# Optimization experiments

Measured on AMD Instinct MI355X. Metric: run time of the kernel, lower is better.

## Reference

```python
import jax, jax.numpy as jnp
import numpy as np

N = 50000      # nodes
E = 800000     # directed edges (before self-loops)
IN = 128       # in_channels
H = 4          # heads (layers 1,2)
C = 64         # hidden_channels per head
OUT = 512      # out_channels of final Linear
LEAKY_SLOPE = 0.2


def _gat_layer(x, src, dst, n, W, a_src, a_dst, b, concat):
    """PyG GATConv (v1): shared linear, additive attention, segment softmax over dst."""
    heads, ch = a_src.shape
    xl = (x @ W).reshape(n, heads, ch)                       # [N,H,C]
    as_n = jnp.sum(xl * a_src, axis=-1)                      # [N,H] alpha_src per node
    ad_n = jnp.sum(xl * a_dst, axis=-1)                      # [N,H] alpha_dst per node
    logits = jax.nn.leaky_relu(as_n[src] + ad_n[dst], LEAKY_SLOPE)  # [Etot,H]
    m = jax.lax.stop_gradient(jax.ops.segment_max(logits, dst, num_segments=n))
    p = jnp.exp(logits - m[dst])
    denom = jax.ops.segment_sum(p, dst, num_segments=n) + 1e-16
    alpha = p / denom[dst]                                   # segment softmax over incoming edges
    out = jax.ops.segment_sum(xl[src] * alpha[:, :, None], dst, num_segments=n)  # [N,H,C]
    out = out.reshape(n, heads * ch) if concat else out.mean(axis=1)
    return out + b


def setup_inputs() -> dict:
    key = jax.random.key(0)
    ks = jax.random.split(key, 16)

    def gl(k, shape, fan_in):
        return jax.random.normal(k, shape, dtype=jnp.float32) * np.float32(1.0 / np.sqrt(fan_in))

    x = jax.random.normal(ks[0], (N, IN), dtype=jnp.float32)
    edge_index = jax.random.randint(ks[1], (2, E), 0, N, dtype=jnp.int32)

    inp = {
        "x": x,
        "edge_index": edge_index,
        # layer 1: in -> H*C (concat)
        "W1": gl(ks[2], (IN, H * C), IN),
        "a_src1": gl(ks[3], (H, C), C),
        "a_dst1": gl(ks[4], (H, C), C),
        "b1": jnp.zeros((H * C,), jnp.float32),
        # layer 2: H*C -> H*C (concat)
        "W2": gl(ks[5], (H * C, H * C), H * C),
        "a_src2": gl(ks[6], (H, C), C),
        "a_dst2": gl(ks[7], (H, C), C),
        "b2": jnp.zeros((H * C,), jnp.float32),
        # layer 3: H*C -> C (1 head, no concat)
        "W3": gl(ks[8], (H * C, C), H * C),
        "a_src3": gl(ks[9], (1, C), C),
        "a_dst3": gl(ks[10], (1, C), C),
        "b3": jnp.zeros((C,), jnp.float32),
        # final fc: C -> OUT
        "Wfc": gl(ks[11], (C, OUT), C),
        "bfc": jnp.zeros((OUT,), jnp.float32),
    }
    return inp


def reference(x, edge_index, W1, a_src1, a_dst1, b1, W2, a_src2, a_dst2, b2,
              W3, a_src3, a_dst3, b3, Wfc, bfc):
    n = x.shape[0]
    loop = jnp.arange(n, dtype=edge_index.dtype)             # PyG GATConv adds self-loops
    src = jnp.concatenate([edge_index[0], loop])
    dst = jnp.concatenate([edge_index[1], loop])

    h = jax.nn.relu(_gat_layer(x, src, dst, n, W1, a_src1, a_dst1, b1, True))
    h = jax.nn.relu(_gat_layer(h, src, dst, n, W2, a_src2, a_dst2, b2, True))
    h = jax.nn.relu(_gat_layer(h, src, dst, n, W3, a_src3, a_dst3, b3, False))
    return jax.nn.relu(h @ Wfc + bfc)                        # [N, OUT]
```

## Files before the change

kernel.cpp:

```cpp
#include <hip/hip_runtime.h>
#include <cstdint>
#include <cstddef>

typedef unsigned short ushort_t;
typedef __bf16 bf16x8 __attribute__((ext_vector_type(8)));
typedef float f32x4 __attribute__((ext_vector_type(4)));

__device__ __forceinline__ float b2f(ushort_t u) {
    return __uint_as_float(((unsigned int)u) << 16);
}
__device__ __forceinline__ ushort_t f2b(float f) {
    __bf16 h = (__bf16)f;
    return *(ushort_t*)&h;
}
__device__ __forceinline__ float lo16(unsigned int u) { return __uint_as_float(u << 16); }
__device__ __forceinline__ float hi16(unsigned int u) { return __uint_as_float(u & 0xffff0000u); }
__device__ __forceinline__ unsigned int pack2(float a, float b) {
    return ((unsigned int)f2b(b) << 16) | (unsigned int)f2b(a);
}

__device__ __forceinline__ void stage8(const float* __restrict__ g, ushort_t* s) {
    float4 f0 = *(const float4*)g;
    float4 f1 = *(const float4*)(g + 4);
    union { ushort_t u[8]; uint4 v; } t;
    t.u[0] = f2b(f0.x); t.u[1] = f2b(f0.y); t.u[2] = f2b(f0.z); t.u[3] = f2b(f0.w);
    t.u[4] = f2b(f1.x); t.u[5] = f2b(f1.y); t.u[6] = f2b(f1.z); t.u[7] = f2b(f1.w);
    *(uint4*)s = t.v;
}
__device__ __forceinline__ void stage8(const ushort_t* __restrict__ g, ushort_t* s) {
    *(float4*)s = *(const float4*)g;
}

__global__ __launch_bounds__(256) void transpose_kernel(const float* __restrict__ W,
                                                        ushort_t* __restrict__ WT,
                                                        int K, int N2) {
    int id = blockIdx.x * 256 + threadIdx.x;
    if (id >= K * N2) return;
    int n = id / K, k = id - n * K;
    WT[id] = f2b(W[k * N2 + n]);
}

__global__ __launch_bounds__(256) void degree_kernel(const int* __restrict__ ei_dst,
                                                     int* __restrict__ deg, int E, int Etot) {
    int e = blockIdx.x * 256 + threadIdx.x;
    if (e >= Etot) return;
    int d = (e < E) ? ei_dst[e] : (e - E);
    atomicAdd(&deg[d], 1);
}

__global__ __launch_bounds__(256) void partial_sum_kernel(const int* __restrict__ deg,
                                                          int* __restrict__ bsum, int n) {
    __shared__ int ws[4];
    int t = threadIdx.x;
    int i = blockIdx.x * 256 + t;
    int v = (i < n) ? deg[i] : 0;
#pragma unroll
    for (int off = 32; off; off >>= 1) v += __shfl_xor(v, off, 64);
    if ((t & 63) == 0) ws[t >> 6] = v;
    __syncthreads();
    if (t == 0) bsum[blockIdx.x] = ws[0] + ws[1] + ws[2] + ws[3];
}

__global__ __launch_bounds__(256) void scan_bsum_kernel(const int* __restrict__ bsum,
                                                        int* __restrict__ boff,
                                                        int* __restrict__ rowoff,
                                                        int nblk, int n) {
    __shared__ int sm[256];
    int t = threadIdx.x;
    int v = (t < nblk) ? bsum[t] : 0;
    sm[t] = v;
    __syncthreads();
#pragma unroll
    for (int off = 1; off < 256; off <<= 1) {
        int u = (t >= off) ? sm[t - off] : 0;
        __syncthreads();
        sm[t] += u;
        __syncthreads();
    }
    if (t < nblk) boff[t] = sm[t] - v;
    if (t == 255) rowoff[n] = sm[255];
}

__global__ __launch_bounds__(256) void block_scan_kernel(const int* __restrict__ deg,
                                                         const int* __restrict__ boff,
                                                         int* __restrict__ rowoff, int n) {
    __shared__ int sm[256];
    int t = threadIdx.x;
    int i = blockIdx.x * 256 + t;
    int v = (i < n) ? deg[i] : 0;
    sm[t] = v;
    __syncthreads();
#pragma unroll
    for (int off = 1; off < 256; off <<= 1) {
        int u = (t >= off) ? sm[t - off] : 0;
        __syncthreads();
        sm[t] += u;
        __syncthreads();
    }
    if (i < n) rowoff[i] = boff[blockIdx.x] + sm[t] - v;
}

__global__ __launch_bounds__(256) void copy_cursor_kernel(const int* __restrict__ rowoff,
                                                          int* __restrict__ cursor, int n) {
    int i = blockIdx.x * 256 + threadIdx.x;
    if (i < n) cursor[i] = rowoff[i];
}

__global__ __launch_bounds__(256) void scatter_kernel(const int* __restrict__ ei_src,
                                                      const int* __restrict__ ei_dst,
                                                      int* __restrict__ cursor,
                                                      int* __restrict__ ssrc, int E, int Etot) {
    int e = blockIdx.x * 256 + threadIdx.x;
    if (e >= Etot) return;
    int s, d;
    if (e < E) { s = ei_src[e]; d = ei_dst[e]; } else { s = d = e - E; }
    int pos = atomicAdd(&cursor[d], 1);
    ssrc[pos] = s;
}

template <typename TA, bool EPI>
__global__ __launch_bounds__(256) void gemm_mfma(const TA* __restrict__ A,
                                                 const ushort_t* __restrict__ WT,
                                                 float* __restrict__ C,
                                                 ushort_t* __restrict__ Cb,
                                                 const float* __restrict__ bias,
                                                 int M, int K, int N2) {
    __shared__ ushort_t sA[64 * 32];
    __shared__ ushort_t sB[64 * 32];
    const int tid = threadIdx.x;
    const int wv = tid >> 6, lane = tid & 63;
    const int quad = lane >> 4, l16 = lane & 15;
    const int bm = blockIdx.x * 64, bn = blockIdx.y * 64;
    const int srow = tid >> 2, skof = (tid & 3) * 8;
    f32x4 acc[4] = {};

    for (int k0 = 0; k0 < K; k0 += 32) {
        int gm = bm + srow;
        gm = gm < M ? gm : M - 1;
        stage8(A + (size_t)gm * K + k0 + skof, sA + srow * 32 + skof);
        stage8(WT + (size_t)(bn + srow) * K + k0 + skof, sB + srow * 32 + skof);
        __syncthreads();

        bf16x8 af = *(const bf16x8*)(sA + (wv * 16 + l16) * 32 + quad * 8);
#pragma unroll
        for (int j = 0; j < 4; j++) {
            bf16x8 bf = *(const bf16x8*)(sB + (j * 16 + l16) * 32 + quad * 8);
            acc[j] = __builtin_amdgcn_mfma_f32_16x16x32_bf16(af, bf, acc[j], 0, 0, 0);
        }
        __syncthreads();
    }

#pragma unroll
    for (int j = 0; j < 4; j++) {
        int col = bn + j * 16 + l16;
        float bv = EPI ? bias[col] : 0.f;
#pragma unroll
        for (int r = 0; r < 4; r++) {
            int row = bm + wv * 16 + quad * 4 + r;
            if (row < M) {
                float v = acc[j][r];
                if (EPI) {
                    v += bv;
                    v = v > 0.f ? v : 0.f;
                    C[(size_t)row * N2 + col] = v;
                } else {
                    Cb[(size_t)row * N2 + col] = f2b(v);
                }
            }
        }
    }
}

template <int CH>
__global__ __launch_bounds__(256) void attn_kernel(const ushort_t* __restrict__ xl,
                                                   const float* __restrict__ a_src,
                                                   const float* __restrict__ a_dst,
                                                   float* __restrict__ as_n,
                                                   float* __restrict__ ad_n, int N) {
    int n = blockIdx.x * 4 + (threadIdx.x >> 6);
    int lane = threadIdx.x & 63;
    if (n >= N) return;
    if (CH == 256) {
        ushort4 u = ((const ushort4*)xl)[(size_t)n * 64 + lane];
        float4 av = ((const float4*)a_src)[lane];
        float4 dv = ((const float4*)a_dst)[lane];
        float x0 = b2f(u.x), x1 = b2f(u.y), x2 = b2f(u.z), x3 = b2f(u.w);
        float s = x0 * av.x + x1 * av.y + x2 * av.z + x3 * av.w;
        float d = x0 * dv.x + x1 * dv.y + x2 * dv.z + x3 * dv.w;
#pragma unroll
        for (int off = 8; off; off >>= 1) {
            s += __shfl_xor(s, off, 64);
            d += __shfl_xor(d, off, 64);
        }
        if ((lane & 15) == 0) {
            int h = lane >> 4;
            as_n[n * 4 + h] = s;
            ad_n[n * 4 + h] = d;
        }
    } else {
        float xv = b2f(xl[(size_t)n * 64 + lane]);
        float s = xv * a_src[lane];
        float d = xv * a_dst[lane];
#pragma unroll
        for (int off = 32; off; off >>= 1) {
            s += __shfl_xor(s, off, 64);
            d += __shfl_xor(d, off, 64);
        }
        if (lane == 0) { as_n[n] = s; ad_n[n] = d; }
    }
}

template <int CH>
__global__ __launch_bounds__(256) void aggregate_kernel(const ushort_t* __restrict__ xl,
                                                        const float* __restrict__ as_n,
                                                        const float* __restrict__ ad_n,
                                                        const int* __restrict__ rowoff,
                                                        const int* __restrict__ ssrc,
                                                        const float* __restrict__ bias,
                                                        ushort_t* __restrict__ hout, int N) {
    const int tid = threadIdx.x;
    const int wv = tid >> 6, lane = tid & 63;
    const uint4* xv = (const uint4*)xl;
    if (CH == 256) {
        const int hw = lane >> 5, l32 = lane & 31;
        const int dd = blockIdx.x * 8 + wv * 2 + hw;
        if (dd >= N) return;
        const int h = l32 >> 3;
        const int r0 = rowoff[dd], r1 = rowoff[dd + 1];
        const float adv = ad_n[dd * 4 + h];
        float a0 = 0, a1 = 0, a2 = 0, a3 = 0, a4 = 0, a5 = 0, a6 = 0, a7 = 0, den = 0;
        for (int i = r0; i < r1; i += 8) {
            int s[8];
            float g[8];
            uint4 u[8];
#pragma unroll
            for (int j = 0; j < 8; j++) {
                int t = i + j;
                s[j] = ssrc[t < r1 ? t : r0];
            }
#pragma unroll
            for (int j = 0; j < 8; j++) g[j] = as_n[s[j] * 4 + h];
#pragma unroll
            for (int j = 0; j < 8; j++) u[j] = xv[(size_t)s[j] * 32 + l32];
#pragma unroll
            for (int j = 0; j < 8; j++) {
                float lg = g[j] + adv;
                lg = lg > 0.f ? lg : 0.2f * lg;
                float p = (i + j < r1) ? __expf(lg) : 0.f;
                den += p;
                a0 += p * lo16(u[j].x); a1 += p * hi16(u[j].x);
                a2 += p * lo16(u[j].y); a3 += p * hi16(u[j].y);
                a4 += p * lo16(u[j].z); a5 += p * hi16(u[j].z);
                a6 += p * lo16(u[j].w); a7 += p * hi16(u[j].w);
            }
        }
        float di = 1.f / (den + 1e-16f);
        float4 b0 = ((const float4*)bias)[l32 * 2];
        float4 b1 = ((const float4*)bias)[l32 * 2 + 1];
        float v0 = a0 * di + b0.x, v1 = a1 * di + b0.y;
        float v2 = a2 * di + b0.z, v3 = a3 * di + b0.w;
        float v4 = a4 * di + b1.x, v5 = a5 * di + b1.y;
        float v6 = a6 * di + b1.z, v7 = a7 * di + b1.w;
        v0 = v0 > 0.f ? v0 : 0.f; v1 = v1 > 0.f ? v1 : 0.f;
        v2 = v2 > 0.f ? v2 : 0.f; v3 = v3 > 0.f ? v3 : 0.f;
        v4 = v4 > 0.f ? v4 : 0.f; v5 = v5 > 0.f ? v5 : 0.f;
        v6 = v6 > 0.f ? v6 : 0.f; v7 = v7 > 0.f ? v7 : 0.f;
        uint4 o;
        o.x = pack2(v0, v1); o.y = pack2(v2, v3);
        o.z = pack2(v4, v5); o.w = pack2(v6, v7);
        ((uint4*)hout)[(size_t)dd * 32 + l32] = o;
    } else {
        const int grp = lane >> 3, l8 = lane & 7;
        const int dd = blockIdx.x * 32 + wv * 8 + grp;
        if (dd >= N) return;
        const int r0 = rowoff[dd], r1 = rowoff[dd + 1];
        const float adv = ad_n[dd];
        float a0 = 0, a1 = 0, a2 = 0, a3 = 0, a4 = 0, a5 = 0, a6 = 0, a7 = 0, den = 0;
        for (int i = r0; i < r1; i += 8) {
            int s[8];
            float g[8];
            uint4 u[8];
#pragma unroll
            for (int j = 0; j < 8; j++) {
                int t = i + j;
                s[j] = ssrc[t < r1 ? t : r0];
            }
#pragma unroll
            for (int j = 0; j < 8; j++) g[j] = as_n[s[j]];
#pragma unroll
            for (int j = 0; j < 8; j++) u[j] = xv[(size_t)s[j] * 8 + l8];
#pragma unroll
            for (int j = 0; j < 8; j++) {
                float lg = g[j] + adv;
                lg = lg > 0.f ? lg : 0.2f * lg;
                float p = (i + j < r1) ? __expf(lg) : 0.f;
                den += p;
                a0 += p * lo16(u[j].x); a1 += p * hi16(u[j].x);
                a2 += p * lo16(u[j].y); a3 += p * hi16(u[j].y);
                a4 += p * lo16(u[j].z); a5 += p * hi16(u[j].z);
                a6 += p * lo16(u[j].w); a7 += p * hi16(u[j].w);
            }
        }
        float di = 1.f / (den + 1e-16f);
        float4 b0 = ((const float4*)bias)[l8 * 2];
        float4 b1 = ((const float4*)bias)[l8 * 2 + 1];
        float v0 = a0 * di + b0.x, v1 = a1 * di + b0.y;
        float v2 = a2 * di + b0.z, v3 = a3 * di + b0.w;
        float v4 = a4 * di + b1.x, v5 = a5 * di + b1.y;
        float v6 = a6 * di + b1.z, v7 = a7 * di + b1.w;
        v0 = v0 > 0.f ? v0 : 0.f; v1 = v1 > 0.f ? v1 : 0.f;
        v2 = v2 > 0.f ? v2 : 0.f; v3 = v3 > 0.f ? v3 : 0.f;
        v4 = v4 > 0.f ? v4 : 0.f; v5 = v5 > 0.f ? v5 : 0.f;
        v6 = v6 > 0.f ? v6 : 0.f; v7 = v7 > 0.f ? v7 : 0.f;
        uint4 o;
        o.x = pack2(v0, v1); o.y = pack2(v2, v3);
        o.z = pack2(v4, v5); o.w = pack2(v6, v7);
        ((uint4*)hout)[(size_t)dd * 8 + l8] = o;
    }
}

extern "C" void kernel_launch(void* const* d_in, const int* in_sizes, int n_in,
                              void* d_out, int out_size, void* d_ws, size_t ws_size,
                              hipStream_t stream) {
    const int N = in_sizes[0] / 128;
    const int E = in_sizes[1] / 2;
    const int Etot = E + N;

    const float* x = (const float*)d_in[0];
    const int* ei = (const int*)d_in[1];
    const int* ei_src = ei;
    const int* ei_dst = ei + E;
    float* out = (float*)d_out;

    const float* as1 = (const float*)d_in[3];
    const float* ad1 = (const float*)d_in[4];
    const float* b1  = (const float*)d_in[5];
    const float* as2 = (const float*)d_in[7];
    const float* ad2 = (const float*)d_in[8];
    const float* b2  = (const float*)d_in[9];
    const float* as3 = (const float*)d_in[11];
    const float* ad3 = (const float*)d_in[12];
    const float* b3  = (const float*)d_in[13];
    const float* bfc = (const float*)d_in[15];

    ushort_t* bufX = (ushort_t*)d_ws;
    ushort_t* bufH = bufX + (size_t)N * 256;
    ushort_t* W1T  = bufH + (size_t)N * 256;
    ushort_t* W2T  = W1T + 32768;
    ushort_t* W3T  = W2T + 65536;
    ushort_t* WfcT = W3T + 16384;
    float* asn = (float*)(WfcT + 32768);
    float* adn = asn + (size_t)N * 4;
    int* deg    = (int*)(adn + (size_t)N * 4);
    int* rowoff = deg + N;
    int* cursor = rowoff + N + 1;
    int* ssrc   = cursor + N;
    int* bsum   = ssrc + Etot;
    int* boff   = bsum + 256;

    transpose_kernel<<<(128 * 256 + 255) / 256, 256, 0, stream>>>((const float*)d_in[2], W1T, 128, 256);
    transpose_kernel<<<(256 * 256 + 255) / 256, 256, 0, stream>>>((const float*)d_in[6], W2T, 256, 256);
    transpose_kernel<<<(256 * 64 + 255) / 256, 256, 0, stream>>>((const float*)d_in[10], W3T, 256, 64);
    transpose_kernel<<<(64 * 512 + 255) / 256, 256, 0, stream>>>((const float*)d_in[14], WfcT, 64, 512);

    hipMemsetAsync(deg, 0, (size_t)N * sizeof(int), stream);
    int eb = (Etot + 255) / 256;
    degree_kernel<<<eb, 256, 0, stream>>>(ei_dst, deg, E, Etot);
    const int NBLK = (N + 255) / 256;
    partial_sum_kernel<<<NBLK, 256, 0, stream>>>(deg, bsum, N);
    scan_bsum_kernel<<<1, 256, 0, stream>>>(bsum, boff, rowoff, NBLK, N);
    block_scan_kernel<<<NBLK, 256, 0, stream>>>(deg, boff, rowoff, N);
    copy_cursor_kernel<<<NBLK, 256, 0, stream>>>(rowoff, cursor, N);
    scatter_kernel<<<eb, 256, 0, stream>>>(ei_src, ei_dst, cursor, ssrc, E, Etot);

    const int MB = (N + 63) / 64;
    int nb4 = (N + 3) / 4;
    int nb8 = (N + 7) / 8;
    int nb32 = (N + 31) / 32;

    gemm_mfma<float, false><<<dim3(MB, 4), 256, 0, stream>>>(x, W1T, nullptr, bufX, nullptr, N, 128, 256);
    attn_kernel<256><<<nb4, 256, 0, stream>>>(bufX, as1, ad1, asn, adn, N);
    aggregate_kernel<256><<<nb8, 256, 0, stream>>>(bufX, asn, adn, rowoff, ssrc, b1, bufH, N);

    gemm_mfma<ushort_t, false><<<dim3(MB, 4), 256, 0, stream>>>(bufH, W2T, nullptr, bufX, nullptr, N, 256, 256);
    attn_kernel<256><<<nb4, 256, 0, stream>>>(bufX, as2, ad2, asn, adn, N);
    aggregate_kernel<256><<<nb8, 256, 0, stream>>>(bufX, asn, adn, rowoff, ssrc, b2, bufH, N);

    gemm_mfma<ushort_t, false><<<dim3(MB, 1), 256, 0, stream>>>(bufH, W3T, nullptr, bufX, nullptr, N, 256, 64);
    attn_kernel<64><<<nb4, 256, 0, stream>>>(bufX, as3, ad3, asn, adn, N);
    aggregate_kernel<64><<<nb32, 256, 0, stream>>>(bufX, asn, adn, rowoff, ssrc, b3, bufH, N);

    gemm_mfma<ushort_t, true><<<dim3(MB, 8), 256, 0, stream>>>(bufH, WfcT, out, nullptr, bfc, N, 64, 512);
}
```

Measured before the change: 496.7 us.

## Aggregate raw inputs before first-layer projection, folding attention vectors into W1

Layer 1 is reordered so that it aggregates the 128-wide bf16 input features per head first, producing a [N,4,128] buffer, and only then applies W1 per head through a GEMM with bias and ReLU fused into its epilogue. The attention logits come from precomputed W1·a_src and W1·a_dst vectors applied to x directly. Per-edge gathers drop from 256 to 128 channels (as 4 heads × 128 after aggregation). In exchange the intermediate buffer doubles in size and the layer-1 GEMM runs per head with an offset A pointer.

```diff
diff --git a/kernel.cpp b/kernel.cpp
--- a/kernel.cpp
+++ b/kernel.cpp
@@ -19,14 +19,6 @@
     return ((unsigned int)f2b(b) << 16) | (unsigned int)f2b(a);
 }
 
-__device__ __forceinline__ void stage8(const float* __restrict__ g, ushort_t* s) {
-    float4 f0 = *(const float4*)g;
-    float4 f1 = *(const float4*)(g + 4);
-    union { ushort_t u[8]; uint4 v; } t;
-    t.u[0] = f2b(f0.x); t.u[1] = f2b(f0.y); t.u[2] = f2b(f0.z); t.u[3] = f2b(f0.w);
-    t.u[4] = f2b(f1.x); t.u[5] = f2b(f1.y); t.u[6] = f2b(f1.z); t.u[7] = f2b(f1.w);
-    *(uint4*)s = t.v;
-}
 __device__ __forceinline__ void stage8(const ushort_t* __restrict__ g, ushort_t* s) {
     *(float4*)s = *(const float4*)g;
 }
@@ -38,6 +30,73 @@
     if (id >= K * N2) return;
     int n = id / K, k = id - n * K;
     WT[id] = f2b(W[k * N2 + n]);
+}
+
+__global__ __launch_bounds__(256) void prep_asad_kernel(const float* __restrict__ W1,
+                                                        const float* __restrict__ a_src,
+                                                        const float* __restrict__ a_dst,
+                                                        float* __restrict__ was,
+                                                        float* __restrict__ wad) {
+#pragma unroll
+    for (int it = 0; it < 4; it++) {
+        int id = it * 256 + threadIdx.x;
+        int side = id >> 9;
+        int rem = id & 511;
+        int h = rem >> 7, c = rem & 127;
+        const float* av = side ? a_dst : a_src;
+        float sum = 0.f;
+#pragma unroll 8
+        for (int k = 0; k < 64; k++) sum += W1[c * 256 + h * 64 + k] * av[h * 64 + k];
+        (side ? wad : was)[h * 128 + c] = sum;
+    }
+}
+
+__global__ __launch_bounds__(256) void xb_kernel(const float* __restrict__ x,
+                                                 ushort_t* __restrict__ xb, int total8) {
+    int id = blockIdx.x * 256 + threadIdx.x;
+    if (id >= total8) return;
+    const float* g = x + (size_t)id * 8;
+    float4 f0 = *(const float4*)g;
+    float4 f1 = *(const float4*)(g + 4);
+    uint4 o;
+    o.x = pack2(f0.x, f0.y); o.y = pack2(f0.z, f0.w);
+    o.z = pack2(f1.x, f1.y); o.w = pack2(f1.z, f1.w);
+    ((uint4*)xb)[id] = o;
+}
+
+__global__ __launch_bounds__(256) void asad_kernel(const ushort_t* __restrict__ xb,
+                                                   const float* __restrict__ was,
+                                                   const float* __restrict__ wad,
+                                                   float* __restrict__ as_n,
+                                                   float* __restrict__ ad_n, int N) {
+    int n = blockIdx.x * 4 + (threadIdx.x >> 6);
+    int lane = threadIdx.x & 63;
+    if (n >= N) return;
+    unsigned int xp = ((const unsigned int*)xb)[(size_t)n * 64 + lane];
+    float x0 = lo16(xp), x1 = hi16(xp);
+    float s[4], d[4];
+#pragma unroll
+    for (int h = 0; h < 4; h++) {
+        float2 wa = ((const float2*)(was + h * 128))[lane];
+        float2 wd = ((const float2*)(wad + h * 128))[lane];
+        s[h] = x0 * wa.x + x1 * wa.y;
+        d[h] = x0 * wd.x + x1 * wd.y;
+    }
+#pragma unroll
+    for (int off = 32; off; off >>= 1) {
+#pragma unroll
+        for (int h = 0; h < 4; h++) {
+            s[h] += __shfl_xor(s[h], off, 64);
+            d[h] += __shfl_xor(d[h], off, 64);
+        }
+    }
+    if (lane == 0) {
+#pragma unroll
+        for (int h = 0; h < 4; h++) {
+            as_n[n * 4 + h] = s[h];
+            ad_n[n * 4 + h] = d[h];
+        }
+    }
 }
 
 __global__ __launch_bounds__(256) void degree_kernel(const int* __restrict__ ei_dst,
@@ -118,26 +177,74 @@
     ssrc[pos] = s;
 }
 
-template <typename TA, bool EPI>
-__global__ __launch_bounds__(256) void gemm_mfma(const TA* __restrict__ A,
+__global__ __launch_bounds__(256) void agg_pre_kernel(const ushort_t* __restrict__ xb,
+                                                      const float* __restrict__ as_n,
+                                                      const float* __restrict__ ad_n,
+                                                      const int* __restrict__ rowoff,
+                                                      const int* __restrict__ ssrc,
+                                                      ushort_t* __restrict__ y, int N) {
+    const int tid = threadIdx.x;
+    const int wv = tid >> 6, lane = tid & 63;
+    const int dd = blockIdx.x * 4 + wv;
+    if (dd >= N) return;
+    const int h = lane >> 4, l16 = lane & 15;
+    const int r0 = rowoff[dd], r1 = rowoff[dd + 1];
+    const float adv = ad_n[dd * 4 + h];
+    const uint4* xv = (const uint4*)xb;
+    float a0 = 0, a1 = 0, a2 = 0, a3 = 0, a4 = 0, a5 = 0, a6 = 0, a7 = 0, den = 0;
+    for (int i = r0; i < r1; i += 8) {
+        int s[8];
+        float g[8];
+        uint4 u[8];
+#pragma unroll
+        for (int j = 0; j < 8; j++) {
+            int t = i + j;
+            s[j] = ssrc[t < r1 ? t : r0];
+        }
+#pragma unroll
+        for (int j = 0; j < 8; j++) g[j] = as_n[s[j] * 4 + h];
+#pragma unroll
+        for (int j = 0; j < 8; j++) u[j] = xv[(size_t)s[j] * 16 + l16];
+#pragma unroll
+        for (int j = 0; j < 8; j++) {
+            float lg = g[j] + adv;
+            lg = lg > 0.f ? lg : 0.2f * lg;
+            float p = (i + j < r1) ? __expf(lg) : 0.f;
+            den += p;
+            a0 += p * lo16(u[j].x); a1 += p * hi16(u[j].x);
+            a2 += p * lo16(u[j].y); a3 += p * hi16(u[j].y);
+            a4 += p * lo16(u[j].z); a5 += p * hi16(u[j].z);
+            a6 += p * lo16(u[j].w); a7 += p * hi16(u[j].w);
+        }
+    }
+    float di = 1.f / (den + 1e-16f);
+    uint4 o;
+    o.x = pack2(a0 * di, a1 * di); o.y = pack2(a2 * di, a3 * di);
+    o.z = pack2(a4 * di, a5 * di); o.w = pack2(a6 * di, a7 * di);
+    ((uint4*)y)[(size_t)dd * 64 + h * 16 + l16] = o;
+}
+
+template <int EPI>
+__global__ __launch_bounds__(256) void gemm_mfma(const ushort_t* __restrict__ A,
                                                  const ushort_t* __restrict__ WT,
                                                  float* __restrict__ C,
                                                  ushort_t* __restrict__ Cb,
                                                  const float* __restrict__ bias,
-                                                 int M, int K, int N2) {
+                                                 int M, int K, int N2, int lda, int aoff_mul) {
     __shared__ ushort_t sA[64 * 32];
     __shared__ ushort_t sB[64 * 32];
     const int tid = threadIdx.x;
     const int wv = tid >> 6, lane = tid & 63;
     const int quad = lane >> 4, l16 = lane & 15;
     const int bm = blockIdx.x * 64, bn = blockIdx.y * 64;
+    const int aoff = blockIdx.y * aoff_mul;
     const int srow = tid >> 2, skof = (tid & 3) * 8;
     f32x4 acc[4] = {};
 
     for (int k0 = 0; k0 < K; k0 += 32) {
         int gm = bm + srow;
         gm = gm < M ? gm : M - 1;
-        stage8(A + (size_t)gm * K + k0 + skof, sA + srow * 32 + skof);
+        stage8(A + (size_t)gm * lda + aoff + k0 + skof, sA + srow * 32 + skof);
         stage8(WT + (size_t)(bn + srow) * K + k0 + skof, sB + srow * 32 + skof);
         __syncthreads();
 
@@ -153,16 +260,20 @@
 #pragma unroll
     for (int j = 0; j < 4; j++) {
         int col = bn + j * 16 + l16;
-        float bv = EPI ? bias[col] : 0.f;
+        float bv = (EPI != 0) ? bias[col] : 0.f;
 #pragma unroll
         for (int r = 0; r < 4; r++) {
             int row = bm + wv * 16 + quad * 4 + r;
             if (row < M) {
                 float v = acc[j][r];
-                if (EPI) {
+                if (EPI == 1) {
                     v += bv;
                     v = v > 0.f ? v : 0.f;
                     C[(size_t)row * N2 + col] = v;
+                } else if (EPI == 2) {
+                    v += bv;
+                    v = v > 0.f ? v : 0.f;
+                    Cb[(size_t)row * N2 + col] = f2b(v);
                 } else {
                     Cb[(size_t)row * N2 + col] = f2b(v);
                 }
@@ -343,25 +454,31 @@
     const float* b3  = (const float*)d_in[13];
     const float* bfc = (const float*)d_in[15];
 
+    ushort_t* bufY = (ushort_t*)d_ws;
     ushort_t* bufX = (ushort_t*)d_ws;
-    ushort_t* bufH = bufX + (size_t)N * 256;
+    ushort_t* bufH = bufY + (size_t)N * 512;
     ushort_t* W1T  = bufH + (size_t)N * 256;
     ushort_t* W2T  = W1T + 32768;
     ushort_t* W3T  = W2T + 65536;
     ushort_t* WfcT = W3T + 16384;
-    float* asn = (float*)(WfcT + 32768);
-    float* adn = asn + (size_t)N * 4;
+    float* was  = (float*)(WfcT + 32768);
+    float* wad  = was + 512;
+    float* asn  = wad + 512;
+    float* adn  = asn + (size_t)N * 4;
     int* deg    = (int*)(adn + (size_t)N * 4);
     int* rowoff = deg + N;
     int* cursor = rowoff + N + 1;
     int* ssrc   = cursor + N;
     int* bsum   = ssrc + Etot;
     int* boff   = bsum + 256;
+    ushort_t* xb = (ushort_t*)(boff + 256);
 
     transpose_kernel<<<(128 * 256 + 255) / 256, 256, 0, stream>>>((const float*)d_in[2], W1T, 128, 256);
     transpose_kernel<<<(256 * 256 + 255) / 256, 256, 0, stream>>>((const float*)d_in[6], W2T, 256, 256);
     transpose_kernel<<<(256 * 64 + 255) / 256, 256, 0, stream>>>((const float*)d_in[10], W3T, 256, 64);
     transpose_kernel<<<(64 * 512 + 255) / 256, 256, 0, stream>>>((const float*)d_in[14], WfcT, 64, 512);
+    prep_asad_kernel<<<1, 256, 0, stream>>>((const float*)d_in[2], as1, ad1, was, wad);
+    xb_kernel<<<(N * 16 + 255) / 256, 256, 0, stream>>>(x, xb, N * 16);
 
     hipMemsetAsync(deg, 0, (size_t)N * sizeof(int), stream);
     int eb = (Etot + 255) / 256;
@@ -378,17 +495,17 @@
     int nb8 = (N + 7) / 8;
     int nb32 = (N + 31) / 32;
 
-    gemm_mfma<float, false><<<dim3(MB, 4), 256, 0, stream>>>(x, W1T, nullptr, bufX, nullptr, N, 128, 256);
-    attn_kernel<256><<<nb4, 256, 0, stream>>>(bufX, as1, ad1, asn, adn, N);
-    aggregate_kernel<256><<<nb8, 256, 0, stream>>>(bufX, asn, adn, rowoff, ssrc, b1, bufH, N);
-
-    gemm_mfma<ushort_t, false><<<dim3(MB, 4), 256, 0, stream>>>(bufH, W2T, nullptr, bufX, nullptr, N, 256, 256);
+    asad_kernel<<<nb4, 256, 0, stream>>>(xb, was, wad, asn, adn, N);
+    agg_pre_kernel<<<nb4, 256, 0, stream>>>(xb, asn, adn, rowoff, ssrc, bufY, N);
+    gemm_mfma<2><<<dim3(MB, 4), 256, 0, stream>>>(bufY, W1T, nullptr, bufH, b1, N, 128, 256, 512, 128);
+
+    gemm_mfma<0><<<dim3(MB, 4), 256, 0, stream>>>(bufH, W2T, nullptr, bufX, nullptr, N, 256, 256, 256, 0);
     attn_kernel<256><<<nb4, 256, 0, stream>>>(bufX, as2, ad2, asn, adn, N);
     aggregate_kernel<256><<<nb8, 256, 0, stream>>>(bufX, asn, adn, rowoff, ssrc, b2, bufH, N);
 
-    gemm_mfma<ushort_t, false><<<dim3(MB, 1), 256, 0, stream>>>(bufH, W3T, nullptr, bufX, nullptr, N, 256, 64);
+    gemm_mfma<0><<<dim3(MB, 1), 256, 0, stream>>>(bufH, W3T, nullptr, bufX, nullptr, N, 256, 64, 256, 0);
     attn_kernel<64><<<nb4, 256, 0, stream>>>(bufX, as3, ad3, asn, adn, N);
     aggregate_kernel<64><<<nb32, 256, 0, stream>>>(bufX, asn, adn, rowoff, ssrc, b3, bufH, N);
 
-    gemm_mfma<ushort_t, true><<<dim3(MB, 8), 256, 0, stream>>>(bufH, WfcT, out, nullptr, bfc, N, 64, 512);
-}
+    gemm_mfma<1><<<dim3(MB, 8), 256, 0, stream>>>(bufH, WfcT, out, nullptr, bfc, N, 64, 512, 64, 0);
+}
```

After: 530.1 us. +6.7%, slower.
